# Optimization experiments

Measured on AMD Instinct MI355X. Metric: run time of the kernel, lower is better.

Reference implementation:

```python
import jax, jax.numpy as jnp
import numpy as np

N = 50000
E = 1600000
F_IN = 256
HEADS = 4
HID = 32
C = 16
NEG_SLOPE = 0.2


def _add_self_loops(edge_index, n):
    loop = jnp.arange(n, dtype=edge_index.dtype)
    return jnp.concatenate([edge_index, jnp.stack([loop, loop])], axis=1)


def gat_conv(x, edge_index, W, att_src, att_dst, bias, heads, n):
    # PyG GATConv (concat=True, add_self_loops=True, inference: no dropout)
    ei = _add_self_loops(edge_index, n)
    src, dst = ei[0], ei[1]
    d = W.shape[1] // heads
    xw = (x @ W).reshape(n, heads, d)                      # [N,H,D]
    a_src = jnp.sum(xw * att_src, axis=-1)                 # [N,H]
    a_dst = jnp.sum(xw * att_dst, axis=-1)                 # [N,H]
    e = jax.nn.leaky_relu(a_src[src] + a_dst[dst], NEG_SLOPE)  # [E',H]
    # segment softmax over destination neighborhoods
    m = jax.ops.segment_max(e, dst, num_segments=n)        # [N,H]
    ex = jnp.exp(e - m[dst])
    denom = jax.ops.segment_sum(ex, dst, num_segments=n)   # [N,H]
    alpha = ex / denom[dst]                                # [E',H]
    msg = xw[src] * alpha[:, :, None]                      # [E',H,D]
    out = jax.ops.segment_sum(msg, dst, num_segments=n)    # [N,H,D]
    return out.reshape(n, heads * d) + bias


def setup_inputs() -> dict:
    key = jax.random.key(0)
    ks = jax.random.split(key, 10)
    g = lambda k, shape, fan: jax.random.normal(k, shape, jnp.float32) * (1.0 / np.sqrt(fan))
    x = jax.random.normal(ks[0], (N, F_IN), jnp.float32)
    edge_index = jax.random.randint(ks[1], (2, E), 0, N, dtype=jnp.int64)
    return {
        "x": x,
        "edge_index": edge_index,
        "W1": g(ks[2], (F_IN, HEADS * HID), F_IN),
        "att_src1": g(ks[3], (HEADS, HID), HID),
        "att_dst1": g(ks[4], (HEADS, HID), HID),
        "b1": jnp.zeros((HEADS * HID,), jnp.float32),
        "W2": g(ks[5], (HEADS * HID, C), HEADS * HID),
        "att_src2": g(ks[6], (1, C), C),
        "att_dst2": g(ks[7], (1, C), C),
        "b2": jnp.zeros((C,), jnp.float32),
    }


def reference(x, edge_index, W1, att_src1, att_dst1, b1, W2, att_src2, att_dst2, b2):
    h = gat_conv(x, edge_index, W1, att_src1, att_dst1, b1, HEADS, N)
    h = jax.nn.relu(h)
    # dropout: identity at inference (training=False)
    out = gat_conv(h, edge_index, W2, att_src2, att_dst2, b2, 1, N)
    return jax.nn.log_softmax(out, axis=1)
```

## Files before the change

kernel.cpp:

```cpp
#include <hip/hip_runtime.h>
#include <hip/hip_bf16.h>

typedef __hip_bfloat16 bf16;
typedef long long i64;
typedef unsigned long long u64;
typedef __attribute__((ext_vector_type(8))) short short8;
typedef __attribute__((ext_vector_type(4))) float floatx4;
typedef __attribute__((ext_vector_type(2))) long long ll2;

#define NN    50000
#define EE    1600000
#define E2    1650000
#define FIN   256
#define HD    128
#define NH    4
#define NC    16
#define SLOPE 0.2f
#define KB    512
#define DPB   98
#define CAPB  4992
#define CAP   4992
#define CH2   2048
#define GBC   782
#define EBC   806

#define KS_S  2312

#define OF_FLAGS 0
#define OF_BCUR  16
#define OF_RP    544
#define OF_W1T   50548
#define OF_BIN   66932
#define OF_CSR   5178740
#define OF_XQ    6828740
#define OF_SC    8428740
#define OF_AS1   8528740
#define OF_AD1   8728740
#define OF_HW2   8928740
#define OF_AS2   9728740
#define OF_AD2   9778740

__device__ __forceinline__ float b2f(bf16 v) { return __bfloat162float(v); }
__device__ __forceinline__ float us2f(unsigned short u) {
    return __uint_as_float(((unsigned)u) << 16);
}
__device__ __forceinline__ unsigned short f2us(float f) {
    unsigned u = __float_as_uint(f);
    return (unsigned short)((u + 0x7fffu + ((u >> 16) & 1u)) >> 16);
}
__device__ __forceinline__ float lrelu(float v) { return v > 0.f ? v : SLOPE * v; }
__device__ __forceinline__ float ub2f(unsigned u, int sh) {
    return (float)((u >> sh) & 0xffu);
}
__device__ __forceinline__ int fwi(int node, int ch) {
    return node * 132 + (ch >> 5) * 33 + (ch & 31);
}

template <bool F32>
__device__ __forceinline__ float ldin(const void* p, int i) {
    if (F32) return ((const float*)p)[i];
    return b2f(((const bf16*)p)[i]);
}
template <bool F32>
__device__ __forceinline__ float4 ldin4(const void* p, int i) {
    if (F32) return *(const float4*)((const float*)p + i);
    ushort4 u = *(const ushort4*)((const unsigned short*)p + i);
    float4 r;
    r.x = us2f(u.x); r.y = us2f(u.y); r.z = us2f(u.z); r.w = us2f(u.w);
    return r;
}

__device__ __forceinline__ void edge_sd(const void* ei, int f64, int e, int& s, int& d) {
    if (e >= EE) { s = e - EE; d = s; return; }
    if (f64) {
        s = (int)((const i64*)ei)[e];
        d = (int)((const i64*)ei)[EE + e];
    } else {
        s = ((const int*)ei)[e];
        d = ((const int*)ei)[EE + e];
    }
    s = min(max(s, 0), NN - 1);
    d = min(max(d, 0), NN - 1);
}

__global__ __launch_bounds__(256) void prep(const void* __restrict__ x,
                                            const void* __restrict__ ei,
                                            const void* __restrict__ W1,
                                            int* __restrict__ flags, int* __restrict__ bcur,
                                            unsigned short* __restrict__ w1t) {
    int t = threadIdx.x;
    const unsigned short* xb = (const unsigned short*)x;
    if (blockIdx.x == 32) {
        __shared__ int cnt[2];
        if (t == 0) { cnt[0] = 0; cnt[1] = 0; }
        bcur[t] = t * CAPB;
        bcur[t + 256] = (t + 256) * CAPB;
        __syncthreads();
        int c0 = 0;
        for (int i = t; i < 4096; i += 256) {
            float v = __uint_as_float(((unsigned)xb[2 * i]) << 16);
            if (!(fabsf(v) < 1e6f)) c0++;
        }
        const i64* e64 = (const i64*)ei;
        int c1 = 0;
        for (int i = t; i < 1024; i += 256) {
            i64 v = e64[i];
            if (v >= 0 && v < NN) c1++;
        }
        atomicAdd(&cnt[0], c0);
        atomicAdd(&cnt[1], c1);
        __syncthreads();
        if (t == 0) {
            flags[0] = (cnt[0] > 400) ? 1 : 0;
            flags[1] = (cnt[1] >= 1000) ? 1 : 0;
        }
        return;
    }
    __shared__ int c0s;
    if (t == 0) c0s = 0;
    __syncthreads();
    int c0 = 0;
    for (int i = t; i < 4096; i += 256) {
        float v = __uint_as_float(((unsigned)xb[2 * i]) << 16);
        if (!(fabsf(v) < 1e6f)) c0++;
    }
    atomicAdd(&c0s, c0);
    __syncthreads();
    bool f32 = c0s > 400;
    int g = blockIdx.x * 256 + t;
    int k = g >> 5, n4 = (g & 31) * 4;
    float4 v = f32 ? ldin4<true>(W1, k * HD + n4) : ldin4<false>(W1, k * HD + n4);
    int ks = k >> 5, kk = k & 31;
    w1t[((ks * HD + n4 + 0) * 32) + kk] = f2us(v.x);
    w1t[((ks * HD + n4 + 1) * 32) + kk] = f2us(v.y);
    w1t[((ks * HD + n4 + 2) * 32) + kk] = f2us(v.z);
    w1t[((ks * HD + n4 + 3) * 32) + kk] = f2us(v.w);
}

template <bool F32>
__global__ __launch_bounds__(256) void gsFuse(
    const void* __restrict__ x, const unsigned short* __restrict__ w1t,
    const void* __restrict__ as1, const void* __restrict__ ad1,
    const void* __restrict__ ei, const int* __restrict__ flags,
    signed char* __restrict__ xq, float* __restrict__ sc2,
    float* __restrict__ asrc, float* __restrict__ adst,
    int* __restrict__ bcur, u64* __restrict__ bin) {
    __shared__ unsigned short af[8 * KS_S];
    __shared__ float scl[128];
    int t = threadIdx.x;

    if (blockIdx.x >= GBC) {
        int* hh  = (int*)af;
        int* res = (int*)af + KB;
        int base = (blockIdx.x - GBC) * CH2 + t * 8;
        hh[t] = 0; hh[t + 256] = 0;
        __syncthreads();
        int f64 = flags[1];
        int sv[8], dv[8], rk[8];
        int n_ = 0;
        if (!f64 && base + 8 <= EE) {
            const int* es = (const int*)ei;
            int4 a = *(const int4*)&es[base];
            int4 b = *(const int4*)&es[base + 4];
            int4 c = *(const int4*)&es[EE + base];
            int4 g = *(const int4*)&es[EE + base + 4];
            sv[0] = a.x; sv[1] = a.y; sv[2] = a.z; sv[3] = a.w;
            sv[4] = b.x; sv[5] = b.y; sv[6] = b.z; sv[7] = b.w;
            dv[0] = c.x; dv[1] = c.y; dv[2] = c.z; dv[3] = c.w;
            dv[4] = g.x; dv[5] = g.y; dv[6] = g.z; dv[7] = g.w;
#pragma unroll
            for (int i = 0; i < 8; i++) {
                sv[i] = min(max(sv[i], 0), NN - 1);
                dv[i] = min(max(dv[i], 0), NN - 1);
            }
            n_ = 8;
        } else if (f64 && base + 8 <= EE) {
            const i64* e64 = (const i64*)ei;
#pragma unroll
            for (int i = 0; i < 4; i++) {
                ll2 sp = *(const ll2*)&e64[base + 2 * i];
                ll2 dp = *(const ll2*)&e64[EE + base + 2 * i];
                sv[2 * i]     = (int)sp[0]; sv[2 * i + 1] = (int)sp[1];
                dv[2 * i]     = (int)dp[0]; dv[2 * i + 1] = (int)dp[1];
            }
#pragma unroll
            for (int i = 0; i < 8; i++) {
                sv[i] = min(max(sv[i], 0), NN - 1);
                dv[i] = min(max(dv[i], 0), NN - 1);
            }
            n_ = 8;
        } else {
            for (int i = 0; i < 8; i++) {
                int e = base + i;
                if (e < E2) {
                    int s, d; edge_sd(ei, f64, e, s, d);
                    sv[n_] = s; dv[n_] = d; n_++;
                }
            }
        }
#pragma unroll 8
        for (int i = 0; i < n_; i++) rk[i] = atomicAdd(&hh[dv[i] / DPB], 1);
        __syncthreads();
        res[t] = hh[t] ? atomicAdd(&bcur[t], hh[t]) : 0;
        res[t + 256] = hh[t + 256] ? atomicAdd(&bcur[t + 256], hh[t + 256]) : 0;
        __syncthreads();
#pragma unroll 8
        for (int i = 0; i < n_; i++) {
            int b = dv[i] / DPB;
            int pos = res[b] + rk[i];
            pos = min(pos, (b + 1) * CAPB - 1);
            bin[pos] = (((u64)(unsigned)dv[i]) << 32) | (unsigned)sv[i];
        }
        return;
    }

    if (flags[0] != (F32 ? 1 : 0)) return;
    int m0 = blockIdx.x * 64;
#pragma unroll
    for (int i = 0; i < 16; i++) {
        int slot = i * 256 + t;
        int mi = slot >> 6, k4 = (slot & 63) * 4;
        float4 v = make_float4(0.f, 0.f, 0.f, 0.f);
        if (m0 + mi < NN) v = ldin4<F32>(x, (m0 + mi) * FIN + k4);
        ushort4 o;
        o.x = f2us(v.x); o.y = f2us(v.y); o.z = f2us(v.z); o.w = f2us(v.w);
        *(ushort4*)&af[(k4 >> 5) * KS_S + mi * 36 + (k4 & 31)] = o;
    }
    __syncthreads();
    int w = t >> 6, lane = t & 63;
    int col = lane & 15, q = lane >> 4;
    floatx4 acc[4][2];
#pragma unroll
    for (int mt = 0; mt < 4; mt++)
#pragma unroll
        for (int u = 0; u < 2; u++) { acc[mt][u].x = 0.f; acc[mt][u].y = 0.f; acc[mt][u].z = 0.f; acc[mt][u].w = 0.f; }
#pragma unroll
    for (int ks = 0; ks < 8; ks++) {
        short8 bf0 = *(const short8*)&w1t[(ks * HD + w * 32 + col) * 32 + q * 8];
        short8 bf1 = *(const short8*)&w1t[(ks * HD + w * 32 + 16 + col) * 32 + q * 8];
#pragma unroll
        for (int mt = 0; mt < 4; mt++) {
            short8 afr = *(const short8*)&af[ks * KS_S + (mt * 16 + col) * 36 + q * 8];
            acc[mt][0] = __builtin_amdgcn_mfma_f32_16x16x32_bf16(afr, bf0, acc[mt][0], 0, 0, 0);
            acc[mt][1] = __builtin_amdgcn_mfma_f32_16x16x32_bf16(afr, bf1, acc[mt][1], 0, 0, 0);
        }
    }
    __syncthreads();
    float* fw = (float*)af;
#pragma unroll
    for (int mt = 0; mt < 4; mt++)
#pragma unroll
        for (int u = 0; u < 2; u++)
#pragma unroll
            for (int r = 0; r < 4; r++) {
                int node = mt * 16 + q * 4 + r;
                fw[fwi(node, w * 32 + u * 16 + col)] = acc[mt][u][r];
            }
    __syncthreads();
    int node = t >> 2, part = t & 3;
    {
        float amax = 0.f;
#pragma unroll
        for (int c = 0; c < 32; c++) amax = fmaxf(amax, fabsf(fw[fwi(node, part * 32 + c)]));
        amax = fmaxf(amax, __shfl_xor(amax, 1));
        if ((part & 1) == 0) {
            scl[node * 2 + (part >> 1)] = (amax > 0.f) ? 127.f / amax : 0.f;
            if (m0 + node < NN) sc2[(m0 + node) * 2 + (part >> 1)] = amax * (1.f / 127.f);
        }
    }
    __syncthreads();
    if (m0 + node < NN) {
        float inv = scl[node * 2 + (part >> 1)];
        unsigned dw[8];
#pragma unroll
        for (int g = 0; g < 8; g++) {
            unsigned pk = 0;
#pragma unroll
            for (int j = 0; j < 4; j++) {
                float v = fw[fwi(node, part * 32 + g * 4 + j)];
                int qi = (int)rintf(v * inv);
                qi = min(127, max(-127, qi));
                pk |= ((unsigned)((qi + 128) & 255)) << (8 * j);
            }
            dw[g] = pk;
        }
        *(uint4*)&xq[(m0 + node) * HD + part * 32]      = make_uint4(dw[0], dw[1], dw[2], dw[3]);
        *(uint4*)&xq[(m0 + node) * HD + part * 32 + 16] = make_uint4(dw[4], dw[5], dw[6], dw[7]);
        float s = 0.f, dd = 0.f;
#pragma unroll
        for (int c = 0; c < 32; c++) {
            float xv = fw[fwi(node, part * 32 + c)];
            s  += xv * ldin<F32>(as1, part * 32 + c);
            dd += xv * ldin<F32>(ad1, part * 32 + c);
        }
        asrc[(m0 + node) * NH + part] = s;
        adst[(m0 + node) * NH + part] = dd;
    }
}

__global__ __launch_bounds__(256) void csrB(const int* __restrict__ bcur,
                                            const u64* __restrict__ bin,
                                            int* __restrict__ rp, int* __restrict__ csr) {
    __shared__ int cnt[512];
    __shared__ int cur[DPB];
    __shared__ int buf[CAP];
    __shared__ int sz[KB];
    __shared__ int sx[256];
    int b = blockIdx.x, t = threadIdx.x;
    sz[t] = min(bcur[t] - t * CAPB, CAPB);
    sz[t + 256] = min(bcur[t + 256] - (t + 256) * CAPB, CAPB);
    __syncthreads();
    int pair = sz[2 * t] + sz[2 * t + 1];
    sx[t] = pair;
    __syncthreads();
    for (int off = 1; off < 256; off <<= 1) {
        int u = (t >= off) ? sx[t - off] : 0;
        __syncthreads();
        sx[t] += u;
        __syncthreads();
    }
    int hp = b >> 1;
    int base = (hp ? sx[hp - 1] : 0) + ((b & 1) ? sz[b & ~1] : 0);
    int size = sz[b];
    if (b == KB - 1 && t == 0) rp[NN] = sx[255];
    int d0 = b * DPB;
    int nd = min(DPB, NN - d0);
    int src0 = b * CAPB;
    cnt[t] = 0; cnt[t + 256] = 0;
    __syncthreads();
    for (int i = t; i < size; i += 256) {
        int d = (int)(bin[src0 + i] >> 32);
        atomicAdd(&cnt[d - d0], 1);
    }
    __syncthreads();
    int a0 = cnt[2 * t], a1 = cnt[2 * t + 1];
    int ps = a0 + a1;
    buf[t] = ps;
    __syncthreads();
    for (int off = 1; off < 256; off <<= 1) {
        int u = (t >= off) ? buf[t - off] : 0;
        __syncthreads();
        buf[t] += u;
        __syncthreads();
    }
    int ex = buf[t] - ps;
    __syncthreads();
    cnt[2 * t] = ex;
    cnt[2 * t + 1] = ex + a0;
    __syncthreads();
    for (int i = t; i < nd; i += 256) {
        rp[d0 + i] = base + cnt[i];
        cur[i] = cnt[i];
    }
    __syncthreads();
    if (size <= CAP) {
        for (int i = t; i < size; i += 256) {
            u64 p = bin[src0 + i];
            int pos = atomicAdd(&cur[(int)(p >> 32) - d0], 1);
            buf[pos] = (int)(unsigned)p;
        }
        __syncthreads();
        for (int i = t; i < size; i += 256) csr[base + i] = buf[i];
    } else {
        for (int i = t; i < size; i += 256) {
            u64 p = bin[src0 + i];
            int pos = base + atomicAdd(&cur[(int)(p >> 32) - d0], 1);
            csr[pos] = (int)(unsigned)p;
        }
    }
}

template <bool F32>
__global__ __launch_bounds__(128) void node1(
    const int* __restrict__ rp, const int* __restrict__ cs,
    const float* __restrict__ asrc, const float* __restrict__ adst,
    const signed char* __restrict__ xq, const float* __restrict__ sc2,
    const void* __restrict__ b1, const void* __restrict__ W2,
    const void* __restrict__ as2, const void* __restrict__ ad2,
    const int* __restrict__ flags, float* __restrict__ hw2,
    float* __restrict__ asrc2, float* __restrict__ adst2) {
    if (flags[0] != (F32 ? 1 : 0)) return;
    int d = blockIdx.x, t = threadIdx.x;
    int beg = rp[d], end = rp[d + 1];
    int deg = end - beg;
    __shared__ float sw[64][4];
    __shared__ int   ss[64];
    __shared__ float red[2][HD];
    __shared__ float wv[2][4];
    __shared__ float hs[HD];
    __shared__ float l2[32];
    int hw_ = t & 3;
    float adw = adst[d * NH + hw_];
    int cg = t & 15, eo = t >> 4, head = cg >> 2;
    float acc[8];
#pragma unroll
    for (int j = 0; j < 8; j++) acc[j] = 0.f;
    float wacc = 0.f, wss = 0.f;
    const unsigned* xqu = (const unsigned*)xq;
    int sl = t >> 2;
    int m = min(deg, 64);
    int nIt = (m + 7) >> 3;
    int ec0 = beg + sl, ec1 = beg + sl + 32;
    int s0 = cs[min(ec0, E2 - 1)];
    int s1 = cs[min(ec1, E2 - 1)];
    int sg[8];
#pragma unroll
    for (int k = 0; k < 8; k++)
        if (k < nIt) sg[k] = cs[min(beg + eo + 8 * k, E2 - 1)];
    float a0 = asrc[s0 * NH + hw_];
    float a1 = asrc[s1 * NH + hw_];
    float q0 = sc2[s0 * 2 + (hw_ >> 1)];
    float q1 = sc2[s1 * 2 + (hw_ >> 1)];
    uint2 uv[8];
#pragma unroll
    for (int k = 0; k < 8; k++)
        if (k < nIt) uv[k] = *(const uint2*)&xqu[sg[k] * 32 + cg * 2];
    float w0 = 0.f, c0 = 0.f, w1 = 0.f, c1 = 0.f;
    if (ec0 < end) { w0 = __expf(fminf(lrelu(a0 + adw), 80.f)); c0 = w0 * q0; }
    if (ec1 < end) { w1 = __expf(fminf(lrelu(a1 + adw), 80.f)); c1 = w1 * q1; }
    sw[sl][hw_] = c0;
    sw[sl + 32][hw_] = c1;
    wacc = w0 + w1;
    __syncthreads();
#pragma unroll
    for (int k = 0; k < 8; k++)
        if (k < nIt) {
            float we = sw[eo + 8 * k][head];
            uint2 u = uv[k];
            acc[0] += we * ub2f(u.x, 0);
            acc[1] += we * ub2f(u.x, 8);
            acc[2] += we * ub2f(u.x, 16);
            acc[3] += we * ub2f(u.x, 24);
            acc[4] += we * ub2f(u.y, 0);
            acc[5] += we * ub2f(u.y, 8);
            acc[6] += we * ub2f(u.y, 16);
            acc[7] += we * ub2f(u.y, 24);
            wss += we;
        }
    for (int chb = beg + 64; chb < end; chb += 32) {
        __syncthreads();
        int ec = chb + sl;
        float w = 0.f, wsc = 0.f;
        int s = 0;
        if (ec < end) {
            s = cs[ec];
            w = __expf(fminf(lrelu(asrc[s * NH + hw_] + adw), 80.f));
            wsc = w * sc2[s * 2 + (hw_ >> 1)];
        }
        sw[sl][hw_] = wsc;
        if (hw_ == 0) ss[sl] = s;
        wacc += w;
        __syncthreads();
        int mm = min(32, end - chb);
        for (int e = eo; e < mm; e += 8) {
            float we = sw[e][head];
            int s2 = ss[e];
            uint2 u = *(const uint2*)&xqu[s2 * 32 + cg * 2];
            acc[0] += we * ub2f(u.x, 0);
            acc[1] += we * ub2f(u.x, 8);
            acc[2] += we * ub2f(u.x, 16);
            acc[3] += we * ub2f(u.x, 24);
            acc[4] += we * ub2f(u.y, 0);
            acc[5] += we * ub2f(u.y, 8);
            acc[6] += we * ub2f(u.y, 16);
            acc[7] += we * ub2f(u.y, 24);
            wss += we;
        }
    }
#pragma unroll
    for (int j = 0; j < 8; j++) acc[j] -= 128.f * wss;
    wacc += __shfl_xor(wacc, 4);
    wacc += __shfl_xor(wacc, 8);
    wacc += __shfl_xor(wacc, 16);
    wacc += __shfl_xor(wacc, 32);
    int wid = t >> 6, lane = t & 63;
    if (lane < 4) wv[wid][lane] = wacc;
#pragma unroll
    for (int j = 0; j < 8; j++) {
        acc[j] += __shfl_xor(acc[j], 16);
        acc[j] += __shfl_xor(acc[j], 32);
    }
    if (lane < 16) {
#pragma unroll
        for (int j = 0; j < 8; j++) red[wid][lane * 8 + j] = acc[j];
    }
    __syncthreads();
    float tot = red[0][t] + red[1][t];
    float wt  = wv[0][t >> 5] + wv[1][t >> 5];
    hs[t] = fmaxf(tot / wt + ldin<F32>(b1, t), 0.f);
    __syncthreads();
    int j = t & 15, g = t >> 4;
    float p = 0.f;
#pragma unroll
    for (int k = 0; k < 16; k++) p += hs[g * 16 + k] * ldin<F32>(W2, (g * 16 + k) * NC + j);
    p += __shfl_xor(p, 16);
    p += __shfl_xor(p, 32);
    if ((t & 63) < 16) l2[(t >> 6) * 16 + j] = p;
    __syncthreads();
    if (t < 16) {
        float hw = l2[t] + l2[16 + t];
        hw2[d * NC + t] = hw;
        float a2s = hw * ldin<F32>(as2, t);
        float a2d = hw * ldin<F32>(ad2, t);
#pragma unroll
        for (int off = 8; off; off >>= 1) {
            a2s += __shfl_xor(a2s, off, 16);
            a2d += __shfl_xor(a2d, off, 16);
        }
        if (t == 0) { asrc2[d] = a2s; adst2[d] = a2d; }
    }
}

template <bool F32>
__global__ __launch_bounds__(256) void node2(
    const int* __restrict__ rp, const int* __restrict__ cs,
    const float* __restrict__ asrc2, const float* __restrict__ adst2,
    const float* __restrict__ hw2, const void* __restrict__ b2,
    const int* __restrict__ flags, void* __restrict__ out) {
    if (flags[0] != (F32 ? 1 : 0)) return;
    int t = threadIdx.x, wid = t >> 6, lane = t & 63;
    int d = blockIdx.x * 4 + wid;
    if (d >= NN) return;
    int beg = rp[d], end = rp[d + 1];
    float ad = adst2[d];
    int q = lane & 3, eo = lane >> 2;
    float4 acc = make_float4(0.f, 0.f, 0.f, 0.f);
    float wtot = 0.f;
    for (int chb = beg; chb < end; chb += 64) {
        int ec = chb + lane;
        int s = 0;
        bool val = ec < end;
        if (val) s = cs[ec];
        int mm = min(64, end - chb);
        int nk = (mm + 15) >> 4;
        float4 v[4];
        int s2a[4];
#pragma unroll
        for (int k = 0; k < 4; k++)
            if (k < nk) s2a[k] = __shfl(s, eo + k * 16);
#pragma unroll
        for (int k = 0; k < 4; k++)
            if (k < nk) v[k] = *(const float4*)&hw2[s2a[k] * NC + q * 4];
        float w = 0.f;
        if (val) w = __expf(fminf(lrelu(asrc2[s] + ad), 80.f));
        float ws = w;
        ws += __shfl_xor(ws, 1);
        ws += __shfl_xor(ws, 2);
        ws += __shfl_xor(ws, 4);
        ws += __shfl_xor(ws, 8);
        ws += __shfl_xor(ws, 16);
        ws += __shfl_xor(ws, 32);
        wtot += ws;
#pragma unroll
        for (int k = 0; k < 4; k++)
            if (k < nk) {
                float we = __shfl(w, eo + k * 16);
                acc.x += we * v[k].x; acc.y += we * v[k].y;
                acc.z += we * v[k].z; acc.w += we * v[k].w;
            }
    }
#pragma unroll
    for (int off = 4; off < 64; off <<= 1) {
        acc.x += __shfl_xor(acc.x, off);
        acc.y += __shfl_xor(acc.y, off);
        acc.z += __shfl_xor(acc.z, off);
        acc.w += __shfl_xor(acc.w, off);
    }
    float rw = 1.f / wtot;
    float v0 = acc.x * rw + ldin<F32>(b2, q * 4 + 0);
    float v1 = acc.y * rw + ldin<F32>(b2, q * 4 + 1);
    float v2 = acc.z * rw + ldin<F32>(b2, q * 4 + 2);
    float v3 = acc.w * rw + ldin<F32>(b2, q * 4 + 3);
    float mx = fmaxf(fmaxf(v0, v1), fmaxf(v2, v3));
    mx = fmaxf(mx, __shfl_xor(mx, 1));
    mx = fmaxf(mx, __shfl_xor(mx, 2));
    float es = __expf(v0 - mx) + __expf(v1 - mx) + __expf(v2 - mx) + __expf(v3 - mx);
    es += __shfl_xor(es, 1);
    es += __shfl_xor(es, 2);
    float lse = mx + __logf(es);
    if (lane < 4) {
        if (F32) {
            *(float4*)&((float*)out)[d * NC + q * 4] =
                make_float4(v0 - lse, v1 - lse, v2 - lse, v3 - lse);
        } else {
            bf16* o = (bf16*)out + d * NC + q * 4;
            o[0] = __float2bfloat16(v0 - lse); o[1] = __float2bfloat16(v1 - lse);
            o[2] = __float2bfloat16(v2 - lse); o[3] = __float2bfloat16(v3 - lse);
        }
    }
}

extern "C" void kernel_launch(void* const* d_in, const int* in_sizes, int n_in,
                              void* d_out, int out_size, void* d_ws, size_t ws_size,
                              hipStream_t stream) {
    const void* x   = d_in[0];
    const void* ei  = d_in[1];
    const void* W1  = d_in[2];
    const void* as1 = d_in[3];
    const void* ad1 = d_in[4];
    const void* b1  = d_in[5];
    const void* W2  = d_in[6];
    const void* as2 = d_in[7];
    const void* ad2 = d_in[8];
    const void* b2v = d_in[9];

    float* ws = (float*)d_ws;
    int* flags = (int*)(ws + OF_FLAGS);
    int* bcur  = (int*)(ws + OF_BCUR);
    int* rp    = (int*)(ws + OF_RP);
    unsigned short* w1t = (unsigned short*)(ws + OF_W1T);
    u64* bin   = (u64*)(ws + OF_BIN);
    int* csr   = (int*)(ws + OF_CSR);
    signed char* xq = (signed char*)(ws + OF_XQ);
    float* sc2   = ws + OF_SC;
    float* asrc1 = ws + OF_AS1;
    float* adst1 = ws + OF_AD1;
    float* hw2   = ws + OF_HW2;
    float* asrc2 = ws + OF_AS2;
    float* adst2 = ws + OF_AD2;

    prep<<<33, 256, 0, stream>>>(x, ei, W1, flags, bcur, w1t);
    gsFuse<true><<<GBC + EBC, 256, 0, stream>>>(x, w1t, as1, ad1, ei, flags, xq, sc2,
                                                asrc1, adst1, bcur, bin);
    csrB<<<KB, 256, 0, stream>>>(bcur, bin, rp, csr);
    node1<true><<<NN, 128, 0, stream>>>(rp, csr, asrc1, adst1, xq, sc2, b1, W2, as2, ad2,
                                        flags, hw2, asrc2, adst2);
    node2<true><<<(NN + 3) / 4, 256, 0, stream>>>(rp, csr, asrc2, adst2, hw2, b2v, flags,
                                                  d_out);
}
```

Measured before the change: 262.1 us.

## Overlap CSR construction with GEMM instead of edge binning

Splits the edge bin-scatter into its own kernel and fuses the per-bin CSR build into the GEMM kernel as extra blocks. The aim is to hide CSR construction latency behind the first-layer projection rather than hiding the scatter. The CSR arrays now reuse the GEMM's shared buffer. Running the scatter serially may cost about as much as it saves.

```diff
diff --git a/kernel.cpp b/kernel.cpp
--- a/kernel.cpp
+++ b/kernel.cpp
@@ -137,79 +137,153 @@
     w1t[((ks * HD + n4 + 3) * 32) + kk] = f2us(v.w);
 }
 
+__global__ __launch_bounds__(256) void binScatter(const void* __restrict__ ei,
+                                                  const int* __restrict__ flags,
+                                                  int* __restrict__ bcur,
+                                                  u64* __restrict__ bin) {
+    __shared__ int hh[KB], res[KB];
+    int t = threadIdx.x;
+    int base = blockIdx.x * CH2 + t * 8;
+    hh[t] = 0; hh[t + 256] = 0;
+    __syncthreads();
+    int f64 = flags[1];
+    int sv[8], dv[8], rk[8];
+    int n_ = 0;
+    if (!f64 && base + 8 <= EE) {
+        const int* es = (const int*)ei;
+        int4 a = *(const int4*)&es[base];
+        int4 b = *(const int4*)&es[base + 4];
+        int4 c = *(const int4*)&es[EE + base];
+        int4 g = *(const int4*)&es[EE + base + 4];
+        sv[0] = a.x; sv[1] = a.y; sv[2] = a.z; sv[3] = a.w;
+        sv[4] = b.x; sv[5] = b.y; sv[6] = b.z; sv[7] = b.w;
+        dv[0] = c.x; dv[1] = c.y; dv[2] = c.z; dv[3] = c.w;
+        dv[4] = g.x; dv[5] = g.y; dv[6] = g.z; dv[7] = g.w;
+#pragma unroll
+        for (int i = 0; i < 8; i++) {
+            sv[i] = min(max(sv[i], 0), NN - 1);
+            dv[i] = min(max(dv[i], 0), NN - 1);
+        }
+        n_ = 8;
+    } else if (f64 && base + 8 <= EE) {
+        const i64* e64 = (const i64*)ei;
+#pragma unroll
+        for (int i = 0; i < 4; i++) {
+            ll2 sp = *(const ll2*)&e64[base + 2 * i];
+            ll2 dp = *(const ll2*)&e64[EE + base + 2 * i];
+            sv[2 * i]     = (int)sp[0]; sv[2 * i + 1] = (int)sp[1];
+            dv[2 * i]     = (int)dp[0]; dv[2 * i + 1] = (int)dp[1];
+        }
+#pragma unroll
+        for (int i = 0; i < 8; i++) {
+            sv[i] = min(max(sv[i], 0), NN - 1);
+            dv[i] = min(max(dv[i], 0), NN - 1);
+        }
+        n_ = 8;
+    } else {
+        for (int i = 0; i < 8; i++) {
+            int e = base + i;
+            if (e < E2) {
+                int s, d; edge_sd(ei, f64, e, s, d);
+                sv[n_] = s; dv[n_] = d; n_++;
+            }
+        }
+    }
+#pragma unroll 8
+    for (int i = 0; i < n_; i++) rk[i] = atomicAdd(&hh[dv[i] / DPB], 1);
+    __syncthreads();
+    res[t] = hh[t] ? atomicAdd(&bcur[t], hh[t]) : 0;
+    res[t + 256] = hh[t + 256] ? atomicAdd(&bcur[t + 256], hh[t + 256]) : 0;
+    __syncthreads();
+#pragma unroll 8
+    for (int i = 0; i < n_; i++) {
+        int b = dv[i] / DPB;
+        int pos = res[b] + rk[i];
+        pos = min(pos, (b + 1) * CAPB - 1);
+        bin[pos] = (((u64)(unsigned)dv[i]) << 32) | (unsigned)sv[i];
+    }
+}
+
 template <bool F32>
-__global__ __launch_bounds__(256) void gsFuse(
+__global__ __launch_bounds__(256) void gcFuse(
     const void* __restrict__ x, const unsigned short* __restrict__ w1t,
     const void* __restrict__ as1, const void* __restrict__ ad1,
-    const void* __restrict__ ei, const int* __restrict__ flags,
+    const int* __restrict__ flags,
     signed char* __restrict__ xq, float* __restrict__ sc2,
     float* __restrict__ asrc, float* __restrict__ adst,
-    int* __restrict__ bcur, u64* __restrict__ bin) {
+    const int* __restrict__ bcur, const u64* __restrict__ bin,
+    int* __restrict__ rp, int* __restrict__ csr) {
     __shared__ unsigned short af[8 * KS_S];
     __shared__ float scl[128];
     int t = threadIdx.x;
 
     if (blockIdx.x >= GBC) {
-        int* hh  = (int*)af;
-        int* res = (int*)af + KB;
-        int base = (blockIdx.x - GBC) * CH2 + t * 8;
-        hh[t] = 0; hh[t + 256] = 0;
-        __syncthreads();
-        int f64 = flags[1];
-        int sv[8], dv[8], rk[8];
-        int n_ = 0;
-        if (!f64 && base + 8 <= EE) {
-            const int* es = (const int*)ei;
-            int4 a = *(const int4*)&es[base];
-            int4 b = *(const int4*)&es[base + 4];
-            int4 c = *(const int4*)&es[EE + base];
-            int4 g = *(const int4*)&es[EE + base + 4];
-            sv[0] = a.x; sv[1] = a.y; sv[2] = a.z; sv[3] = a.w;
-            sv[4] = b.x; sv[5] = b.y; sv[6] = b.z; sv[7] = b.w;
-            dv[0] = c.x; dv[1] = c.y; dv[2] = c.z; dv[3] = c.w;
-            dv[4] = g.x; dv[5] = g.y; dv[6] = g.z; dv[7] = g.w;
-#pragma unroll
-            for (int i = 0; i < 8; i++) {
-                sv[i] = min(max(sv[i], 0), NN - 1);
-                dv[i] = min(max(dv[i], 0), NN - 1);
+        int* cnt = (int*)af;
+        int* cur = cnt + 512;
+        int* buf = cur + DPB;
+        int* sz  = buf + CAP;
+        int* sx  = sz + KB;
+        int b = blockIdx.x - GBC;
+        sz[t] = min(bcur[t] - t * CAPB, CAPB);
+        sz[t + 256] = min(bcur[t + 256] - (t + 256) * CAPB, CAPB);
+        __syncthreads();
+        int pair = sz[2 * t] + sz[2 * t + 1];
+        sx[t] = pair;
+        __syncthreads();
+        for (int off = 1; off < 256; off <<= 1) {
+            int u = (t >= off) ? sx[t - off] : 0;
+            __syncthreads();
+            sx[t] += u;
+            __syncthreads();
+        }
+        int hp = b >> 1;
+        int base = (hp ? sx[hp - 1] : 0) + ((b & 1) ? sz[b & ~1] : 0);
+        int size = sz[b];
+        if (b == KB - 1 && t == 0) rp[NN] = sx[255];
+        int d0 = b * DPB;
+        int nd = min(DPB, NN - d0);
+        int src0 = b * CAPB;
+        cnt[t] = 0; cnt[t + 256] = 0;
+        __syncthreads();
+        for (int i = t; i < size; i += 256) {
+            int d = (int)(bin[src0 + i] >> 32);
+            atomicAdd(&cnt[d - d0], 1);
+        }
+        __syncthreads();
+        int a0 = cnt[2 * t], a1 = cnt[2 * t + 1];
+        int ps = a0 + a1;
+        buf[t] = ps;
+        __syncthreads();
+        for (int off = 1; off < 256; off <<= 1) {
+            int u = (t >= off) ? buf[t - off] : 0;
+            __syncthreads();
+            buf[t] += u;
+            __syncthreads();
+        }
+        int ex = buf[t] - ps;
+        __syncthreads();
+        cnt[2 * t] = ex;
+        cnt[2 * t + 1] = ex + a0;
+        __syncthreads();
+        for (int i = t; i < nd; i += 256) {
+            rp[d0 + i] = base + cnt[i];
+            cur[i] = cnt[i];
+        }
+        __syncthreads();
+        if (size <= CAP) {
+            for (int i = t; i < size; i += 256) {
+                u64 p = bin[src0 + i];
+                int pos = atomicAdd(&cur[(int)(p >> 32) - d0], 1);
+                buf[pos] = (int)(unsigned)p;
             }
-            n_ = 8;
-        } else if (f64 && base + 8 <= EE) {
-            const i64* e64 = (const i64*)ei;
-#pragma unroll
-            for (int i = 0; i < 4; i++) {
-                ll2 sp = *(const ll2*)&e64[base + 2 * i];
-                ll2 dp = *(const ll2*)&e64[EE + base + 2 * i];
-                sv[2 * i]     = (int)sp[0]; sv[2 * i + 1] = (int)sp[1];
-                dv[2 * i]     = (int)dp[0]; dv[2 * i + 1] = (int)dp[1];
+            __syncthreads();
+            for (int i = t; i < size; i += 256) csr[base + i] = buf[i];
+        } else {
+            for (int i = t; i < size; i += 256) {
+                u64 p = bin[src0 + i];
+                int pos = base + atomicAdd(&cur[(int)(p >> 32) - d0], 1);
+                csr[pos] = (int)(unsigned)p;
             }
-#pragma unroll
-            for (int i = 0; i < 8; i++) {
-                sv[i] = min(max(sv[i], 0), NN - 1);
-                dv[i] = min(max(dv[i], 0), NN - 1);
-            }
-            n_ = 8;
-        } else {
-            for (int i = 0; i < 8; i++) {
-                int e = base + i;
-                if (e < E2) {
-                    int s, d; edge_sd(ei, f64, e, s, d);
-                    sv[n_] = s; dv[n_] = d; n_++;
-                }
-            }
-        }
-#pragma unroll 8
-        for (int i = 0; i < n_; i++) rk[i] = atomicAdd(&hh[dv[i] / DPB], 1);
-        __syncthreads();
-        res[t] = hh[t] ? atomicAdd(&bcur[t], hh[t]) : 0;
-        res[t + 256] = hh[t + 256] ? atomicAdd(&bcur[t + 256], hh[t + 256]) : 0;
-        __syncthreads();
-#pragma unroll 8
-        for (int i = 0; i < n_; i++) {
-            int b = dv[i] / DPB;
-            int pos = res[b] + rk[i];
-            pos = min(pos, (b + 1) * CAPB - 1);
-            bin[pos] = (((u64)(unsigned)dv[i]) << 32) | (unsigned)sv[i];
         }
         return;
     }
@@ -295,78 +369,6 @@
         }
         asrc[(m0 + node) * NH + part] = s;
         adst[(m0 + node) * NH + part] = dd;
-    }
-}
-
-__global__ __launch_bounds__(256) void csrB(const int* __restrict__ bcur,
-                                            const u64* __restrict__ bin,
-                                            int* __restrict__ rp, int* __restrict__ csr) {
-    __shared__ int cnt[512];
-    __shared__ int cur[DPB];
-    __shared__ int buf[CAP];
-    __shared__ int sz[KB];
-    __shared__ int sx[256];
-    int b = blockIdx.x, t = threadIdx.x;
-    sz[t] = min(bcur[t] - t * CAPB, CAPB);
-    sz[t + 256] = min(bcur[t + 256] - (t + 256) * CAPB, CAPB);
-    __syncthreads();
-    int pair = sz[2 * t] + sz[2 * t + 1];
-    sx[t] = pair;
-    __syncthreads();
-    for (int off = 1; off < 256; off <<= 1) {
-        int u = (t >= off) ? sx[t - off] : 0;
-        __syncthreads();
-        sx[t] += u;
-        __syncthreads();
-    }
-    int hp = b >> 1;
-    int base = (hp ? sx[hp - 1] : 0) + ((b & 1) ? sz[b & ~1] : 0);
-    int size = sz[b];
-    if (b == KB - 1 && t == 0) rp[NN] = sx[255];
-    int d0 = b * DPB;
-    int nd = min(DPB, NN - d0);
-    int src0 = b * CAPB;
-    cnt[t] = 0; cnt[t + 256] = 0;
-    __syncthreads();
-    for (int i = t; i < size; i += 256) {
-        int d = (int)(bin[src0 + i] >> 32);
-        atomicAdd(&cnt[d - d0], 1);
-    }
-    __syncthreads();
-    int a0 = cnt[2 * t], a1 = cnt[2 * t + 1];
-    int ps = a0 + a1;
-    buf[t] = ps;
-    __syncthreads();
-    for (int off = 1; off < 256; off <<= 1) {
-        int u = (t >= off) ? buf[t - off] : 0;
-        __syncthreads();
-        buf[t] += u;
-        __syncthreads();
-    }
-    int ex = buf[t] - ps;
-    __syncthreads();
-    cnt[2 * t] = ex;
-    cnt[2 * t + 1] = ex + a0;
-    __syncthreads();
-    for (int i = t; i < nd; i += 256) {
-        rp[d0 + i] = base + cnt[i];
-        cur[i] = cnt[i];
-    }
-    __syncthreads();
-    if (size <= CAP) {
-        for (int i = t; i < size; i += 256) {
-            u64 p = bin[src0 + i];
-            int pos = atomicAdd(&cur[(int)(p >> 32) - d0], 1);
-            buf[pos] = (int)(unsigned)p;
-        }
-        __syncthreads();
-        for (int i = t; i < size; i += 256) csr[base + i] = buf[i];
-    } else {
-        for (int i = t; i < size; i += 256) {
-            u64 p = bin[src0 + i];
-            int pos = base + atomicAdd(&cur[(int)(p >> 32) - d0], 1);
-            csr[pos] = (int)(unsigned)p;
-        }
     }
 }
 
@@ -620,9 +622,9 @@
     float* adst2 = ws + OF_AD2;
 
     prep<<<33, 256, 0, stream>>>(x, ei, W1, flags, bcur, w1t);
-    gsFuse<true><<<GBC + EBC, 256, 0, stream>>>(x, w1t, as1, ad1, ei, flags, xq, sc2,
-                                                asrc1, adst1, bcur, bin);
-    csrB<<<KB, 256, 0, stream>>>(bcur, bin, rp, csr);
+    binScatter<<<EBC, 256, 0, stream>>>(ei, flags, bcur, bin);
+    gcFuse<true><<<GBC + KB, 256, 0, stream>>>(x, w1t, as1, ad1, flags, xq, sc2,
+                                               asrc1, adst1, bcur, bin, rp, csr);
     node1<true><<<NN, 128, 0, stream>>>(rp, csr, asrc1, adst1, xq, sc2, b1, W2, as2, ad2,
                                         flags, hw2, asrc2, adst2);
     node2<true><<<(NN + 3) / 4, 256, 0, stream>>>(rp, csr, asrc2, adst2, hw2, b2v, flags,
```

Result: slower. 267.4 us (+2.0%).
